# Kernel optimization log

Hardware: AMD Instinct MI355X
Metric: run time of the kernel (lower is better)

The kernel has to match this reference:

```python
import jax, jax.numpy as jnp
import numpy as np

D_MODEL = 2048
NHEAD = 32
N_KV = 8
HEAD_DIM = D_MODEL // NHEAD
EPS = 1e-5


def setup_inputs() -> dict:
    key = jax.random.key(0)
    k1, k2, k3, k4, k5 = jax.random.split(key, 5)
    B, S = 2, 2048
    return {
        "x": jax.random.normal(k1, (B, S, D_MODEL), dtype=jnp.float32),
        "wq": jax.random.normal(k2, (D_MODEL, D_MODEL), dtype=jnp.float32) * 0.02,
        "wk": jax.random.normal(k3, (N_KV * HEAD_DIM, D_MODEL), dtype=jnp.float32) * 0.02,
        "wv": jax.random.normal(k4, (N_KV * HEAD_DIM, D_MODEL), dtype=jnp.float32) * 0.02,
        "wo": jax.random.normal(k5, (D_MODEL, D_MODEL), dtype=jnp.float32) * 0.02,
    }


def weight_quant(w):
    # ternary/binary quant with straight-through estimator
    scale = jnp.maximum(jnp.mean(jnp.abs(w)), EPS)
    return jax.lax.stop_gradient(jnp.sign(w) * scale - w) + w


def bitlinear(x, w):
    # F.linear(x, weight_quant(w)) = x @ w_q.T
    return x @ weight_quant(w).T


def reference(x, wq, wk, wv, wo):
    B, S, _ = x.shape
    G = NHEAD // N_KV  # kv groups
    # projections
    q = bitlinear(x, wq).reshape(B, S, N_KV, G, HEAD_DIM)   # [B,S,Kv,G,D]
    k = bitlinear(x, wk).reshape(B, S, N_KV, HEAD_DIM)      # [B,S,Kv,D]
    v = bitlinear(x, wv).reshape(B, S, N_KV, HEAD_DIM)
    # GQA causal attention without materializing repeated K/V
    sm_scale = 1.0 / jnp.sqrt(jnp.asarray(HEAD_DIM, dtype=x.dtype))
    scores = jnp.einsum('bskgd,btkd->bkgst', q, k) * sm_scale  # [B,Kv,G,S,S]
    causal = jnp.tril(jnp.ones((S, S), dtype=bool))
    scores = jnp.where(causal, scores, jnp.asarray(-jnp.inf, dtype=scores.dtype))
    probs = jax.nn.softmax(scores, axis=-1)
    out = jnp.einsum('bkgst,btkd->bskgd', probs, v)  # [B,S,Kv,G,D]
    out = out.reshape(B, S, D_MODEL)
    return bitlinear(out, wo)
```

## Files before the change

kernel.cpp:

```cpp
#include <hip/hip_runtime.h>
#include <stdint.h>


#define D_MODEL 2048
#define S_LEN   2048
#define BATCH   2
#define NKV     8
#define HD      64
#define MROWS   (BATCH * S_LEN)
#define NQKV    3072
#define LDQKV   3072

typedef unsigned short u16;
typedef __bf16 bf16x8 __attribute__((ext_vector_type(8)));
typedef float  f32x4  __attribute__((ext_vector_type(4)));

__device__ __forceinline__ u16 f2bf(float f) {
  union { float f; unsigned u; } v; v.f = f;
  unsigned r = v.u + 0x7FFFu + ((v.u >> 16) & 1u);
  return (u16)(r >> 16);
}

__device__ __forceinline__ float exp2_fast(float x) {
  float r; asm("v_exp_f32 %0, %1" : "=v"(r) : "v"(x)); return r;
}

__device__ __forceinline__ unsigned cvt_pk_bf16(float a, float b) {
  unsigned r;
  asm("v_cvt_pk_bf16_f32 %0, %1, %2" : "=v"(r) : "v"(a), "v"(b));
  return r;
}

__device__ __forceinline__ void lds_load16(u16* lds, const u16* g) {
  __builtin_amdgcn_global_load_lds(
      (const __attribute__((address_space(1))) void*)g,
      (__attribute__((address_space(3))) void*)lds, 16, 0, 0);
}

#define SM_LOG2E 0.180336880f
#define THR_LOG2 11.5415603f

__global__ void prep_all(const float* __restrict__ wq, const float* __restrict__ wk,
                         const float* __restrict__ wv, const float* __restrict__ wo,
                         const float* __restrict__ x,
                         u16* __restrict__ wqkvs, u16* __restrict__ wos,
                         u16* __restrict__ xb, double* __restrict__ partials) {
  const int bid = blockIdx.x;
  const float* src; u16* dst; int n4, rb, nb; bool sgn = true;
  if (bid < 256)      { src = wq; dst = wqkvs;                  n4 = 1048576; rb = bid;       nb = 256; }
  else if (bid < 320) { src = wk; dst = wqkvs + 2048 * D_MODEL; n4 = 262144;  rb = bid - 256; nb = 64;  }
  else if (bid < 384) { src = wv; dst = wqkvs + 2560 * D_MODEL; n4 = 262144;  rb = bid - 320; nb = 64;  }
  else if (bid < 640) { src = wo; dst = wos;                    n4 = 1048576; rb = bid - 384; nb = 256; }
  else                { src = x;  dst = xb;                     n4 = 2097152; rb = bid - 640; nb = 512; sgn = false; }

  if (sgn) {
    double s = 0.0;
    for (int i = rb * 256 + threadIdx.x; i < n4; i += nb * 256) {
      float4 v = reinterpret_cast<const float4*>(src)[i];
      ushort4 o;
      o.x = v.x > 0.f ? 0x3F80 : (v.x < 0.f ? 0xBF80 : 0);
      o.y = v.y > 0.f ? 0x3F80 : (v.y < 0.f ? 0xBF80 : 0);
      o.z = v.z > 0.f ? 0x3F80 : (v.z < 0.f ? 0xBF80 : 0);
      o.w = v.w > 0.f ? 0x3F80 : (v.w < 0.f ? 0xBF80 : 0);
      reinterpret_cast<ushort4*>(dst)[i] = o;
      s += (double)fabsf(v.x) + (double)fabsf(v.y) +
           (double)fabsf(v.z) + (double)fabsf(v.w);
    }
    __shared__ double sm[256];
    sm[threadIdx.x] = s;
    __syncthreads();
    for (int off = 128; off > 0; off >>= 1) {
      if (threadIdx.x < off) sm[threadIdx.x] += sm[threadIdx.x + off];
      __syncthreads();
    }
    if (threadIdx.x == 0) partials[bid] = sm[0];
  } else {
    for (int i = rb * 256 + threadIdx.x; i < n4; i += nb * 256) {
      float4 v = reinterpret_cast<const float4*>(src)[i];
      ushort4 o;
      o.x = f2bf(v.x); o.y = f2bf(v.y); o.z = f2bf(v.z); o.w = f2bf(v.w);
      reinterpret_cast<ushort4*>(dst)[i] = o;
    }
  }
}

__global__ void finalize_scales(const double* __restrict__ partials,
                                float* __restrict__ tabs) {
  __shared__ float sc_sh[4];
  const int w = threadIdx.x >> 6;
  const int lane = threadIdx.x & 63;
  const int beg[4] = {0, 256, 320, 384};
  const int cnt[4] = {256, 64, 64, 256};
  const double counts[4] = {4194304.0, 1048576.0, 1048576.0, 4194304.0};
  double s = 0.0;
  for (int i = lane; i < cnt[w]; i += 64) s += partials[beg[w] + i];
  for (int off = 1; off < 64; off <<= 1) s += __shfl_xor(s, off);
  if (lane == 0) sc_sh[w] = fmaxf((float)(s / counts[w]), 1e-5f);
  __syncthreads();
  if (threadIdx.x == 0) {
    const float s0 = sc_sh[0], s1 = sc_sh[1], s2 = sc_sh[2], s3 = sc_sh[3];
    for (int i = 0; i < 24; ++i)
      tabs[i] = (i < 16) ? s0 * SM_LOG2E : (i < 20 ? s1 : s2);
    for (int i = 0; i < 16; ++i) tabs[24 + i] = s3;
  }
}

template <int OUT_BF16, int VSPLIT>
__global__ __launch_bounds__(256, 4) void gemm_bt(
    const u16* __restrict__ A, const u16* __restrict__ Bt, void* __restrict__ Cv,
    const float* __restrict__ tab, u16* __restrict__ vt, int M, int N, int K) {
  __shared__ u16 lA[128 * 64];
  __shared__ u16 lB[128 * 64];
  const int tid = threadIdx.x;
  const int lane = tid & 63, wave = tid >> 6;
  const int lo = lane & 15, hi = lane >> 4;
  const int m0 = blockIdx.y * 128, n0 = blockIdx.x * 128;
  const int wr = (wave >> 1) * 64, wc = (wave & 1) * 64;

  f32x4 acc[4][4] = {};

  for (int k0 = 0; k0 < K; k0 += 64) {
#pragma unroll
    for (int it = 0; it < 4; ++it) {
      const int c = it * 256 + wave * 64 + lane;
      const int row = c >> 3, kc = (c & 7) << 3;
      lds_load16(&lA[(it * 256 + wave * 64) * 8], &A[(size_t)(m0 + row) * K + k0 + kc]);
      lds_load16(&lB[(it * 256 + wave * 64) * 8], &Bt[(size_t)(n0 + row) * K + k0 + kc]);
    }
    __syncthreads();
#pragma unroll
    for (int kk = 0; kk < 2; ++kk) {
      bf16x8 af[4], bfr[4];
#pragma unroll
      for (int i = 0; i < 4; ++i)
        af[i] = *reinterpret_cast<const bf16x8*>(&lA[(wr + i * 16 + lo) * 64 + kk * 32 + hi * 8]);
#pragma unroll
      for (int i = 0; i < 4; ++i)
        bfr[i] = *reinterpret_cast<const bf16x8*>(&lB[(wc + i * 16 + lo) * 64 + kk * 32 + hi * 8]);
#pragma unroll
      for (int mi = 0; mi < 4; ++mi)
#pragma unroll
        for (int ni = 0; ni < 4; ++ni)
          acc[mi][ni] = __builtin_amdgcn_mfma_f32_16x16x32_bf16(af[mi], bfr[ni], acc[mi][ni], 0, 0, 0);
    }
    __syncthreads();
  }

  const float scale = tab[blockIdx.x];
  if (VSPLIT && (int)blockIdx.x >= 20) {
#pragma unroll
    for (int mi = 0; mi < 4; ++mi) {
#pragma unroll
      for (int ni = 0; ni < 4; ++ni) {
        const int col = (n0 - 2560) + wc + ni * 16 + lo;
        const int row = m0 + wr + mi * 16 + hi * 4;
        unsigned w01 = (unsigned)f2bf(acc[mi][ni][0] * scale) |
                       ((unsigned)f2bf(acc[mi][ni][1] * scale) << 16);
        unsigned w23 = (unsigned)f2bf(acc[mi][ni][2] * scale) |
                       ((unsigned)f2bf(acc[mi][ni][3] * scale) << 16);
        uint2 pk; pk.x = w01; pk.y = w23;
        *reinterpret_cast<uint2*>(vt + (size_t)col * MROWS + row) = pk;
      }
    }
    return;
  }
#pragma unroll
  for (int mi = 0; mi < 4; ++mi) {
#pragma unroll
    for (int ni = 0; ni < 4; ++ni) {
#pragma unroll
      for (int r = 0; r < 4; ++r) {
        const int row = m0 + wr + mi * 16 + hi * 4 + r;
        const int col = n0 + wc + ni * 16 + lo;
        const float v = acc[mi][ni][r] * scale;
        if (OUT_BF16)
          reinterpret_cast<u16*>(Cv)[(size_t)row * N + col] = f2bf(v);
        else
          reinterpret_cast<float*>(Cv)[(size_t)row * N + col] = v;
      }
    }
  }
}

__device__ __forceinline__ void stage_tile(u16* dst, const u16* base, int ld,
                                           int tid, int wave) {
#pragma unroll
  for (int it = 0; it < 2; ++it) {
    const int c = it * 256 + tid;
    const int row = c >> 3;
    const int ch = (c & 7) ^ (row & 7);
    lds_load16(dst + (it * 256 + wave * 64) * 8, base + (size_t)row * ld + ch * 8);
  }
}

#define TILE_BODY(MASKED)                                                      \
  {                                                                            \
    const int t0 = ti * 64;                                                    \
    const int cur = ti & 1;                                                    \
    u16* lKc = (u16*)lK[cur];                                                  \
    u16* lVc = (u16*)lV[cur];                                                  \
    if (ti + 1 < nt) {                                                         \
      stage_tile(lK[cur ^ 1], Kb + (size_t)(brow + t0 + 64) * LDQKV, LDQKV,    \
                 tid, wave);                                                   \
      stage_tile(lV[cur ^ 1], Vb + t0 + 64, MROWS, tid, wave);                 \
    }                                                                          \
    f32x4 sacc[2][4] = {};                                                     \
    __builtin_amdgcn_s_setprio(1);                                             \
    _Pragma("unroll")                                                          \
    for (int kk = 0; kk < 2; ++kk) {                                           \
      _Pragma("unroll")                                                        \
      for (int nf = 0; nf < 4; ++nf) {                                         \
        bf16x8 kf = *reinterpret_cast<const bf16x8*>(                          \
            &lKc[(nf * 16 + lo) * 64 + ((kk * 32 + hi * 8) ^ swl)]);           \
        _Pragma("unroll")                                                      \
        for (int mi = 0; mi < 2; ++mi)                                         \
          sacc[mi][nf] = __builtin_amdgcn_mfma_f32_16x16x32_bf16(              \
              kf, qf[mi][kk], sacc[mi][nf], 0, 0, 0);                          \
      }                                                                        \
    }                                                                          \
    __builtin_amdgcn_s_setprio(0);                                             \
    float rowmax[2];                                                           \
    bool ok = true;                                                            \
    _Pragma("unroll")                                                          \
    for (int mi = 0; mi < 2; ++mi) {                                           \
      if (MASKED) {                                                            \
        const int qg = q0w + mi * 16 + lo;                                     \
        _Pragma("unroll")                                                      \
        for (int nf = 0; nf < 4; ++nf) {                                       \
          _Pragma("unroll")                                                    \
          for (int r = 0; r < 4; ++r) {                                        \
            const int tg = t0 + nf * 16 + hi * 4 + r;                          \
            if (tg > qg) sacc[mi][nf][r] = -1e30f;                             \
          }                                                                    \
        }                                                                      \
      }                                                                        \
      float mnf[4];                                                            \
      _Pragma("unroll")                                                        \
      for (int nf = 0; nf < 4; ++nf)                                           \
        mnf[nf] = fmaxf(fmaxf(sacc[mi][nf][0], sacc[mi][nf][1]),               \
                        fmaxf(sacc[mi][nf][2], sacc[mi][nf][3]));              \
      float mt = fmaxf(fmaxf(mnf[0], mnf[1]), fmaxf(mnf[2], mnf[3]));          \
      mt = fmaxf(mt, __shfl_xor(mt, 16));                                      \
      mt = fmaxf(mt, __shfl_xor(mt, 32));                                      \
      rowmax[mi] = mt;                                                         \
      ok = ok && (mt <= m_run[mi] + THR_LOG2);                                 \
    }                                                                          \
    if (!__all((int)ok)) {                                                     \
      _Pragma("unroll")                                                        \
      for (int mi = 0; mi < 2; ++mi) {                                         \
        const float mn = fmaxf(m_run[mi], rowmax[mi]);                         \
        const float alpha = exp2_fast(m_run[mi] - mn);                         \
        m_run[mi] = mn;                                                        \
        l_lane[mi] *= alpha;                                                   \
        const float a0 = __shfl(alpha, xbase + 0);                             \
        const float a1 = __shfl(alpha, xbase + 1);                             \
        const float a2 = __shfl(alpha, xbase + 2);                             \
        const float a3 = __shfl(alpha, xbase + 3);                             \
        _Pragma("unroll")                                                      \
        for (int nf = 0; nf < 4; ++nf) {                                       \
          oacc[mi][nf][0] *= a0; oacc[mi][nf][1] *= a1;                        \
          oacc[mi][nf][2] *= a2; oacc[mi][nf][3] *= a3;                        \
        }                                                                      \
      }                                                                        \
    }                                                                          \
    _Pragma("unroll")                                                          \
    for (int mi = 0; mi < 2; ++mi) {                                           \
      u16* lprow = &lP[wave][(mi * 16 + lo) * 72 + hi * 4];                    \
      float ls = 0.f;                                                          \
      _Pragma("unroll")                                                        \
      for (int nf = 0; nf < 4; ++nf) {                                         \
        const float e0 = exp2_fast(sacc[mi][nf][0] - m_run[mi]);               \
        const float e1 = exp2_fast(sacc[mi][nf][1] - m_run[mi]);               \
        const float e2 = exp2_fast(sacc[mi][nf][2] - m_run[mi]);               \
        const float e3 = exp2_fast(sacc[mi][nf][3] - m_run[mi]);               \
        ls += (e0 + e1) + (e2 + e3);                                           \
        uint2 pk; pk.x = cvt_pk_bf16(e0, e1); pk.y = cvt_pk_bf16(e2, e3);      \
        *reinterpret_cast<uint2*>(lprow + nf * 16) = pk;                       \
      }                                                                        \
      l_lane[mi] += ls;                                                        \
    }                                                                          \
    __builtin_amdgcn_s_setprio(1);                                             \
    _Pragma("unroll")                                                          \
    for (int kk = 0; kk < 2; ++kk) {                                           \
      bf16x8 pf[2];                                                            \
      _Pragma("unroll")                                                        \
      for (int mi = 0; mi < 2; ++mi)                                           \
        pf[mi] = *reinterpret_cast<const bf16x8*>(                             \
            &lP[wave][(mi * 16 + lo) * 72 + kk * 32 + hi * 8]);                \
      _Pragma("unroll")                                                        \
      for (int nf = 0; nf < 4; ++nf) {                                         \
        bf16x8 vf = *reinterpret_cast<const bf16x8*>(                          \
            &lVc[(nf * 16 + lo) * 64 + ((kk * 32 + hi * 8) ^ swl)]);           \
        _Pragma("unroll")                                                      \
        for (int mi = 0; mi < 2; ++mi)                                         \
          oacc[mi][nf] = __builtin_amdgcn_mfma_f32_16x16x32_bf16(              \
              pf[mi], vf, oacc[mi][nf], 0, 0, 0);                              \
      }                                                                        \
    }                                                                          \
    __builtin_amdgcn_s_setprio(0);                                             \
    __syncthreads();                                                           \
  }

__global__ __launch_bounds__(256, 2) void flash_attn(
    const u16* __restrict__ QKV, const u16* __restrict__ VT,
    u16* __restrict__ Og) {
  __shared__ u16 lK[2][64 * 64];
  __shared__ u16 lV[2][64 * 64];
  __shared__ u16 lP[4][32 * 72];

  const int tid = threadIdx.x;
  const int lane = tid & 63, wave = tid >> 6;
  const int lo = lane & 15, hi = lane >> 4;
  const int lin = (int)blockIdx.y * 8 + (int)blockIdx.x;
  const int xcd = lin & 7, slot = lin >> 3;
  const int G = xcd * 2 + (slot >> 5);
  const int wb = slot & 31;
  const int b = G >> 3, kv = G & 7;
  const int h = kv * 4 + (wb >> 3);
  const int lbx = wb & 7;
  const int brow = b * S_LEN;
  const u16* Q  = QKV + h * HD;
  const u16* Kb = QKV + 2048 + kv * HD;
  const u16* Vb = VT + (size_t)(kv * HD) * MROWS + brow;
  const int swl = (lo & 7) << 3;
  const int xbase = (lane & 48) | ((lane >> 2) & 12);

#pragma unroll 1
  for (int pi = 0; pi < 2; ++pi) {
    const int qt = pi == 0 ? lbx : (15 - lbx);
    const int q0 = qt * 128;
    const int q0w = q0 + wave * 32;
    const int nt = 2 * qt + 2;

    bf16x8 qf[2][2];
#pragma unroll
    for (int mi = 0; mi < 2; ++mi) {
      const size_t qr = (size_t)(brow + q0w + mi * 16 + lo) * LDQKV;
#pragma unroll
      for (int kk = 0; kk < 2; ++kk)
        qf[mi][kk] = *reinterpret_cast<const bf16x8*>(&Q[qr + kk * 32 + hi * 8]);
    }

    f32x4 oacc[2][4] = {};
    float m_run[2] = {-1e30f, -1e30f};
    float l_lane[2] = {0.f, 0.f};

    stage_tile(lK[0], Kb + (size_t)brow * LDQKV, LDQKV, tid, wave);
    stage_tile(lV[0], Vb, MROWS, tid, wave);
    __syncthreads();

#pragma unroll 1
    for (int ti = 0; ti < 2 * qt; ++ti) TILE_BODY(0)
#pragma unroll 1
    for (int ti = 2 * qt; ti < nt; ++ti) TILE_BODY(1)

#pragma unroll
    for (int mi = 0; mi < 2; ++mi) {
      float ls = l_lane[mi];
      ls += __shfl_xor(ls, 16);
      ls += __shfl_xor(ls, 32);
      const float inv = 1.f / ls;
      const float i0 = __shfl(inv, xbase + 0);
      const float i1 = __shfl(inv, xbase + 1);
      const float i2 = __shfl(inv, xbase + 2);
      const float i3 = __shfl(inv, xbase + 3);
#pragma unroll
      for (int nf = 0; nf < 4; ++nf) {
        const size_t rb0 = (size_t)(brow + q0w + mi * 16 + hi * 4) * D_MODEL +
                           h * HD + nf * 16 + lo;
        Og[rb0 + 0 * D_MODEL] = f2bf(oacc[mi][nf][0] * i0);
        Og[rb0 + 1 * D_MODEL] = f2bf(oacc[mi][nf][1] * i1);
        Og[rb0 + 2 * D_MODEL] = f2bf(oacc[mi][nf][2] * i2);
        Og[rb0 + 3 * D_MODEL] = f2bf(oacc[mi][nf][3] * i3);
      }
    }
  }
}

extern "C" void kernel_launch(void* const* d_in, const int* in_sizes, int n_in,
                              void* d_out, int out_size, void* d_ws, size_t ws_size,
                              hipStream_t stream) {
  (void)in_sizes; (void)n_in; (void)out_size; (void)ws_size;
  const float* x  = (const float*)d_in[0];
  const float* wq = (const float*)d_in[1];
  const float* wk = (const float*)d_in[2];
  const float* wv = (const float*)d_in[3];
  const float* wo = (const float*)d_in[4];
  float* out = (float*)d_out;
  char* ws = (char*)d_ws;

  double* partials = (double*)ws;
  float* tabs = (float*)(ws + 6144);
  size_t off = 8192;
  u16* xb    = (u16*)(ws + off); off += (size_t)MROWS * D_MODEL * 2;
  u16* wqkvs = (u16*)(ws + off); off += (size_t)NQKV * D_MODEL * 2;
  u16* wos   = (u16*)(ws + off); off += (size_t)D_MODEL * D_MODEL * 2;
  u16* qkvb  = (u16*)(ws + off); off += (size_t)MROWS * NQKV * 2;
  u16* ao    = (u16*)(ws + off); off += (size_t)MROWS * D_MODEL * 2;
  u16* vt    = (u16*)(ws + off); off += (size_t)512 * MROWS * 2;

  prep_all<<<1152, 256, 0, stream>>>(wq, wk, wv, wo, x, wqkvs, wos, xb, partials);
  finalize_scales<<<1, 256, 0, stream>>>(partials, tabs);

  gemm_bt<1, 1><<<dim3(NQKV / 128, MROWS / 128), 256, 0, stream>>>(
      xb, wqkvs, qkvb, tabs, vt, MROWS, NQKV, D_MODEL);

  flash_attn<<<dim3(8, 64), 256, 0, stream>>>(qkvb, vt, ao);

  gemm_bt<0, 0><<<dim3(D_MODEL / 128, MROWS / 128), 256, 0, stream>>>(
      ao, wos, out, tabs + 24, nullptr, MROWS, D_MODEL, D_MODEL);
}
```

Baseline: 195.9 us.

## Switch attention to 32x32x16 MFMA with transposed S and register-resident P

Rewrites the flash-attention tile body to use 32x32x16 bf16 MFMAs computing S^T, so each lane owns one query row. The rowmax and rescale now need only a single cross-half shuffle, and alpha no longer has to be broadcast per lane. P is repacked in registers with v_permlane32_swap instead of a round trip through LDS, which removes the lP buffer. The next-tile prefetch now starts after the QK MFMAs, and the output is written as packed 8-byte stores. The larger f32x16 accumulators raise register pressure, which may hurt occupancy at two blocks per CU.

```diff
diff --git a/kernel.cpp b/kernel.cpp
--- a/kernel.cpp
+++ b/kernel.cpp
@@ -14,6 +14,8 @@
 typedef unsigned short u16;
 typedef __bf16 bf16x8 __attribute__((ext_vector_type(8)));
 typedef float  f32x4  __attribute__((ext_vector_type(4)));
+typedef float  f32x16 __attribute__((ext_vector_type(16)));
+typedef unsigned u32x4 __attribute__((ext_vector_type(4)));
 
 __device__ __forceinline__ u16 f2bf(float f) {
   union { float f; unsigned u; } v; v.f = f;
@@ -199,102 +201,82 @@
     const int cur = ti & 1;                                                    \
     u16* lKc = (u16*)lK[cur];                                                  \
     u16* lVc = (u16*)lV[cur];                                                  \
+    f32x16 sacc[2] = {};                                                       \
+    __builtin_amdgcn_s_setprio(1);                                             \
+    _Pragma("unroll")                                                          \
+    for (int w = 0; w < 4; ++w) {                                              \
+      _Pragma("unroll")                                                        \
+      for (int nf = 0; nf < 2; ++nf) {                                         \
+        bf16x8 kf = *reinterpret_cast<const bf16x8*>(                          \
+            &lKc[(nf * 32 + q31) * 64 + ((w * 16 + hi5 * 8) ^ swl)]);          \
+        sacc[nf] = __builtin_amdgcn_mfma_f32_32x32x16_bf16(                    \
+            kf, qf[w], sacc[nf], 0, 0, 0);                                     \
+      }                                                                        \
+    }                                                                          \
+    __builtin_amdgcn_s_setprio(0);                                             \
     if (ti + 1 < nt) {                                                         \
       stage_tile(lK[cur ^ 1], Kb + (size_t)(brow + t0 + 64) * LDQKV, LDQKV,    \
                  tid, wave);                                                   \
       stage_tile(lV[cur ^ 1], Vb + t0 + 64, MROWS, tid, wave);                 \
     }                                                                          \
-    f32x4 sacc[2][4] = {};                                                     \
+    if (MASKED) {                                                              \
+      _Pragma("unroll")                                                        \
+      for (int nf = 0; nf < 2; ++nf) {                                         \
+        _Pragma("unroll")                                                      \
+        for (int rg = 0; rg < 16; ++rg) {                                      \
+          const int tg = t0 + nf * 32 + (rg >> 2) * 8 + hi5 * 4 + (rg & 3);    \
+          if (tg > qg) sacc[nf][rg] = -1e30f;                                  \
+        }                                                                      \
+      }                                                                        \
+    }                                                                          \
+    float mt = -1e30f;                                                         \
+    _Pragma("unroll")                                                          \
+    for (int nf = 0; nf < 2; ++nf) {                                           \
+      _Pragma("unroll")                                                        \
+      for (int rg = 0; rg < 16; ++rg) mt = fmaxf(mt, sacc[nf][rg]);            \
+    }                                                                          \
+    mt = fmaxf(mt, __shfl_xor(mt, 32));                                        \
+    if (!__all((int)(mt <= m_run + THR_LOG2))) {                               \
+      const float mn = fmaxf(m_run, mt);                                       \
+      const float alpha = exp2_fast(m_run - mn);                               \
+      m_run = mn;                                                              \
+      l_lane *= alpha;                                                         \
+      _Pragma("unroll")                                                        \
+      for (int nf = 0; nf < 2; ++nf) {                                         \
+        _Pragma("unroll")                                                      \
+        for (int rg = 0; rg < 16; ++rg) oacc[nf][rg] *= alpha;                 \
+      }                                                                        \
+    }                                                                          \
+    unsigned pk[2][8];                                                         \
+    _Pragma("unroll")                                                          \
+    for (int nf = 0; nf < 2; ++nf) {                                           \
+      _Pragma("unroll")                                                        \
+      for (int c = 0; c < 4; ++c) {                                            \
+        const float e0 = exp2_fast(sacc[nf][4 * c + 0] - m_run);               \
+        const float e1 = exp2_fast(sacc[nf][4 * c + 1] - m_run);               \
+        const float e2 = exp2_fast(sacc[nf][4 * c + 2] - m_run);               \
+        const float e3 = exp2_fast(sacc[nf][4 * c + 3] - m_run);               \
+        l_lane += (e0 + e1) + (e2 + e3);                                       \
+        pk[nf][2 * c + 0] = cvt_pk_bf16(e0, e1);                               \
+        pk[nf][2 * c + 1] = cvt_pk_bf16(e2, e3);                               \
+      }                                                                        \
+    }                                                                          \
     __builtin_amdgcn_s_setprio(1);                                             \
     _Pragma("unroll")                                                          \
-    for (int kk = 0; kk < 2; ++kk) {                                           \
-      _Pragma("unroll")                                                        \
-      for (int nf = 0; nf < 4; ++nf) {                                         \
-        bf16x8 kf = *reinterpret_cast<const bf16x8*>(                          \
-            &lKc[(nf * 16 + lo) * 64 + ((kk * 32 + hi * 8) ^ swl)]);           \
-        _Pragma("unroll")                                                      \
-        for (int mi = 0; mi < 2; ++mi)                                         \
-          sacc[mi][nf] = __builtin_amdgcn_mfma_f32_16x16x32_bf16(              \
-              kf, qf[mi][kk], sacc[mi][nf], 0, 0, 0);                          \
-      }                                                                        \
-    }                                                                          \
-    __builtin_amdgcn_s_setprio(0);                                             \
-    float rowmax[2];                                                           \
-    bool ok = true;                                                            \
-    _Pragma("unroll")                                                          \
-    for (int mi = 0; mi < 2; ++mi) {                                           \
-      if (MASKED) {                                                            \
-        const int qg = q0w + mi * 16 + lo;                                     \
-        _Pragma("unroll")                                                      \
-        for (int nf = 0; nf < 4; ++nf) {                                       \
-          _Pragma("unroll")                                                    \
-          for (int r = 0; r < 4; ++r) {                                        \
-            const int tg = t0 + nf * 16 + hi * 4 + r;                          \
-            if (tg > qg) sacc[mi][nf][r] = -1e30f;                             \
-          }                                                                    \
-        }                                                                      \
-      }                                                                        \
-      float mnf[4];                                                            \
-      _Pragma("unroll")                                                        \
-      for (int nf = 0; nf < 4; ++nf)                                           \
-        mnf[nf] = fmaxf(fmaxf(sacc[mi][nf][0], sacc[mi][nf][1]),               \
-                        fmaxf(sacc[mi][nf][2], sacc[mi][nf][3]));              \
-      float mt = fmaxf(fmaxf(mnf[0], mnf[1]), fmaxf(mnf[2], mnf[3]));          \
-      mt = fmaxf(mt, __shfl_xor(mt, 16));                                      \
-      mt = fmaxf(mt, __shfl_xor(mt, 32));                                      \
-      rowmax[mi] = mt;                                                         \
-      ok = ok && (mt <= m_run[mi] + THR_LOG2);                                 \
-    }                                                                          \
-    if (!__all((int)ok)) {                                                     \
-      _Pragma("unroll")                                                        \
-      for (int mi = 0; mi < 2; ++mi) {                                         \
-        const float mn = fmaxf(m_run[mi], rowmax[mi]);                         \
-        const float alpha = exp2_fast(m_run[mi] - mn);                         \
-        m_run[mi] = mn;                                                        \
-        l_lane[mi] *= alpha;                                                   \
-        const float a0 = __shfl(alpha, xbase + 0);                             \
-        const float a1 = __shfl(alpha, xbase + 1);                             \
-        const float a2 = __shfl(alpha, xbase + 2);                             \
-        const float a3 = __shfl(alpha, xbase + 3);                             \
-        _Pragma("unroll")                                                      \
-        for (int nf = 0; nf < 4; ++nf) {                                       \
-          oacc[mi][nf][0] *= a0; oacc[mi][nf][1] *= a1;                        \
-          oacc[mi][nf][2] *= a2; oacc[mi][nf][3] *= a3;                        \
-        }                                                                      \
-      }                                                                        \
-    }                                                                          \
-    _Pragma("unroll")                                                          \
-    for (int mi = 0; mi < 2; ++mi) {                                           \
-      u16* lprow = &lP[wave][(mi * 16 + lo) * 72 + hi * 4];                    \
-      float ls = 0.f;                                                          \
-      _Pragma("unroll")                                                        \
-      for (int nf = 0; nf < 4; ++nf) {                                         \
-        const float e0 = exp2_fast(sacc[mi][nf][0] - m_run[mi]);               \
-        const float e1 = exp2_fast(sacc[mi][nf][1] - m_run[mi]);               \
-        const float e2 = exp2_fast(sacc[mi][nf][2] - m_run[mi]);               \
-        const float e3 = exp2_fast(sacc[mi][nf][3] - m_run[mi]);               \
-        ls += (e0 + e1) + (e2 + e3);                                           \
-        uint2 pk; pk.x = cvt_pk_bf16(e0, e1); pk.y = cvt_pk_bf16(e2, e3);      \
-        *reinterpret_cast<uint2*>(lprow + nf * 16) = pk;                       \
-      }                                                                        \
-      l_lane[mi] += ls;                                                        \
-    }                                                                          \
-    __builtin_amdgcn_s_setprio(1);                                             \
-    _Pragma("unroll")                                                          \
-    for (int kk = 0; kk < 2; ++kk) {                                           \
-      bf16x8 pf[2];                                                            \
-      _Pragma("unroll")                                                        \
-      for (int mi = 0; mi < 2; ++mi)                                           \
-        pf[mi] = *reinterpret_cast<const bf16x8*>(                             \
-            &lP[wave][(mi * 16 + lo) * 72 + kk * 32 + hi * 8]);                \
-      _Pragma("unroll")                                                        \
-      for (int nf = 0; nf < 4; ++nf) {                                         \
+    for (int w = 0; w < 4; ++w) {                                              \
+      const int nf = w >> 1, c4 = (w & 1) * 4;                                 \
+      unsigned a0 = pk[nf][c4 + 0], a1 = pk[nf][c4 + 1];                       \
+      unsigned b0 = pk[nf][c4 + 2], b1 = pk[nf][c4 + 3];                       \
+      asm volatile("v_permlane32_swap_b32 %0, %1" : "+v"(a0), "+v"(b0));       \
+      asm volatile("v_permlane32_swap_b32 %0, %1" : "+v"(a1), "+v"(b1));       \
+      u32x4 pw; pw.x = a0; pw.y = a1; pw.z = b0; pw.w = b1;                    \
+      bf16x8 pfr = *reinterpret_cast<const bf16x8*>(&pw);                      \
+      _Pragma("unroll")                                                        \
+      for (int nfo = 0; nfo < 2; ++nfo) {                                      \
         bf16x8 vf = *reinterpret_cast<const bf16x8*>(                          \
-            &lVc[(nf * 16 + lo) * 64 + ((kk * 32 + hi * 8) ^ swl)]);           \
-        _Pragma("unroll")                                                      \
-        for (int mi = 0; mi < 2; ++mi)                                         \
-          oacc[mi][nf] = __builtin_amdgcn_mfma_f32_16x16x32_bf16(              \
-              pf[mi], vf, oacc[mi][nf], 0, 0, 0);                              \
+            &lVc[(nfo * 32 + q31) * 64 + ((w * 16 + hi5 * 8) ^ swl)]);         \
+        oacc[nfo] = __builtin_amdgcn_mfma_f32_32x32x16_bf16(                   \
+            vf, pfr, oacc[nfo], 0, 0, 0);                                      \
       }                                                                        \
     }                                                                          \
     __builtin_amdgcn_s_setprio(0);                                             \
@@ -306,11 +288,10 @@
     u16* __restrict__ Og) {
   __shared__ u16 lK[2][64 * 64];
   __shared__ u16 lV[2][64 * 64];
-  __shared__ u16 lP[4][32 * 72];
 
   const int tid = threadIdx.x;
   const int lane = tid & 63, wave = tid >> 6;
-  const int lo = lane & 15, hi = lane >> 4;
+  const int q31 = lane & 31, hi5 = lane >> 5;
   const int lin = (int)blockIdx.y * 8 + (int)blockIdx.x;
   const int xcd = lin & 7, slot = lin >> 3;
   const int G = xcd * 2 + (slot >> 5);
@@ -322,8 +303,7 @@
   const u16* Q  = QKV + h * HD;
   const u16* Kb = QKV + 2048 + kv * HD;
   const u16* Vb = VT + (size_t)(kv * HD) * MROWS + brow;
-  const int swl = (lo & 7) << 3;
-  const int xbase = (lane & 48) | ((lane >> 2) & 12);
+  const int swl = (lane & 7) << 3;
 
 #pragma unroll 1
   for (int pi = 0; pi < 2; ++pi) {
@@ -331,19 +311,18 @@
     const int q0 = qt * 128;
     const int q0w = q0 + wave * 32;
     const int nt = 2 * qt + 2;
-
-    bf16x8 qf[2][2];
-#pragma unroll
-    for (int mi = 0; mi < 2; ++mi) {
-      const size_t qr = (size_t)(brow + q0w + mi * 16 + lo) * LDQKV;
-#pragma unroll
-      for (int kk = 0; kk < 2; ++kk)
-        qf[mi][kk] = *reinterpret_cast<const bf16x8*>(&Q[qr + kk * 32 + hi * 8]);
-    }
-
-    f32x4 oacc[2][4] = {};
-    float m_run[2] = {-1e30f, -1e30f};
-    float l_lane[2] = {0.f, 0.f};
+    const int qg = q0w + q31;
+
+    bf16x8 qf[4];
+    {
+      const size_t qr = (size_t)(brow + q0w + q31) * LDQKV;
+#pragma unroll
+      for (int w = 0; w < 4; ++w)
+        qf[w] = *reinterpret_cast<const bf16x8*>(&Q[qr + w * 16 + hi5 * 8]);
+    }
+
+    f32x16 oacc[2] = {};
+    float m_run = -1e30f, l_lane = 0.f;
 
     stage_tile(lK[0], Kb + (size_t)brow * LDQKV, LDQKV, tid, wave);
     stage_tile(lV[0], Vb, MROWS, tid, wave);
@@ -354,24 +333,23 @@
 #pragma unroll 1
     for (int ti = 2 * qt; ti < nt; ++ti) TILE_BODY(1)
 
-#pragma unroll
-    for (int mi = 0; mi < 2; ++mi) {
-      float ls = l_lane[mi];
-      ls += __shfl_xor(ls, 16);
+    {
+      float ls = l_lane;
       ls += __shfl_xor(ls, 32);
       const float inv = 1.f / ls;
-      const float i0 = __shfl(inv, xbase + 0);
-      const float i1 = __shfl(inv, xbase + 1);
-      const float i2 = __shfl(inv, xbase + 2);
-      const float i3 = __shfl(inv, xbase + 3);
-#pragma unroll
-      for (int nf = 0; nf < 4; ++nf) {
-        const size_t rb0 = (size_t)(brow + q0w + mi * 16 + hi * 4) * D_MODEL +
-                           h * HD + nf * 16 + lo;
-        Og[rb0 + 0 * D_MODEL] = f2bf(oacc[mi][nf][0] * i0);
-        Og[rb0 + 1 * D_MODEL] = f2bf(oacc[mi][nf][1] * i1);
-        Og[rb0 + 2 * D_MODEL] = f2bf(oacc[mi][nf][2] * i2);
-        Og[rb0 + 3 * D_MODEL] = f2bf(oacc[mi][nf][3] * i3);
+#pragma unroll
+      for (int nfo = 0; nfo < 2; ++nfo) {
+#pragma unroll
+        for (int c = 0; c < 4; ++c) {
+          const unsigned u0 = cvt_pk_bf16(oacc[nfo][4 * c + 0] * inv,
+                                          oacc[nfo][4 * c + 1] * inv);
+          const unsigned u1 = cvt_pk_bf16(oacc[nfo][4 * c + 2] * inv,
+                                          oacc[nfo][4 * c + 3] * inv);
+          const int d = nfo * 32 + c * 8 + hi5 * 4;
+          uint2 st; st.x = u0; st.y = u1;
+          *reinterpret_cast<uint2*>(
+              &Og[(size_t)(brow + q0w + q31) * D_MODEL + h * HD + d]) = st;
+        }
       }
     }
   }
```

New measurement: 185.3 us. 5.4% less time.
